# Optimization experiments

Measured on AMD Instinct MI355X. Metric: run time of the kernel, lower is better.

Reference implementation:

```python
import jax, jax.numpy as jnp
import numpy as np
from jax import lax

DN = ('NHWC', 'HWIO', 'NHWC')


def _conv(x, w, b=None, stride=1):
    y = lax.conv_general_dilated(x, w, (stride, stride), 'SAME', dimension_numbers=DN)
    return y + b if b is not None else y


def _conv_t(x, w, b, stride=2):
    y = lax.conv_transpose(x, w, (stride, stride), 'SAME', dimension_numbers=DN)
    return y + b


def _res_stack(x, blocks):
    # ResidualBlock: x + Conv1x1(relu(Conv3x3(relu(x)))); final relu after stack
    for w1, w2 in blocks:
        t = jax.nn.relu(x)
        t = _conv(t, w1)          # 3x3, no bias
        t = jax.nn.relu(t)
        t = _conv(t, w2)          # 1x1, no bias
        x = x + t
    return jax.nn.relu(x)


def setup_inputs() -> dict:
    key = jax.random.key(0)
    ks = jax.random.split(key, 32)
    s = 0.05
    n = lambda i, shape: jax.random.normal(ks[i], shape, dtype=jnp.float32) * s
    H, RH, D, K = 128, 32, 128, 512
    return {
        'x': jax.random.normal(ks[0], (16, 256, 256, 3), dtype=jnp.float32),
        'emb': jax.random.normal(ks[1], (K, D), dtype=jnp.float32),  # stddev 1.0 init
        'enc_w1': n(2, (4, 4, 3, H // 2)),  'enc_b1': jnp.zeros((H // 2,), jnp.float32),
        'enc_w2': n(3, (4, 4, H // 2, H)),  'enc_b2': jnp.zeros((H,), jnp.float32),
        'enc_w3': n(4, (3, 3, H, H)),       'enc_b3': jnp.zeros((H,), jnp.float32),
        'erb1_w1': n(5, (3, 3, H, RH)), 'erb1_w2': n(6, (1, 1, RH, H)),
        'erb2_w1': n(7, (3, 3, H, RH)), 'erb2_w2': n(8, (1, 1, RH, H)),
        'dec_w': n(9, (3, 3, D, H)),        'dec_b': jnp.zeros((H,), jnp.float32),
        'drb1_w1': n(10, (3, 3, H, RH)), 'drb1_w2': n(11, (1, 1, RH, H)),
        'drb2_w1': n(12, (3, 3, H, RH)), 'drb2_w2': n(13, (1, 1, RH, H)),
        'dt1_w': n(14, (4, 4, H, H // 2)),  'dt1_b': jnp.zeros((H // 2,), jnp.float32),
        'dt2_w': n(15, (4, 4, H // 2, 3)),  'dt2_b': jnp.zeros((3,), jnp.float32),
    }


def _forward(x, emb, enc_w1, enc_b1, enc_w2, enc_b2, enc_w3, enc_b3,
             erb1_w1, erb1_w2, erb2_w1, erb2_w2,
             dec_w, dec_b, drb1_w1, drb1_w2, drb2_w1, drb2_w2,
             dt1_w, dt1_b, dt2_w, dt2_b):
    f = jax.nn.relu(_conv(x, enc_w1, enc_b1, 2))
    f = jax.nn.relu(_conv(f, enc_w2, enc_b2, 2))
    f = _conv(f, enc_w3, enc_b3, 1)
    f = _res_stack(f, [(erb1_w1, erb1_w2), (erb2_w1, erb2_w2)])
    # VQ: full [N, K] squared-distance matrix, argmin, codebook gather
    D = emb.shape[1]
    flat = f.reshape(-1, D)                                   # [N, D]
    dist = ((flat ** 2).sum(axis=1, keepdims=True)
            + (emb ** 2).sum(axis=1)[None, :]
            - 2.0 * flat @ emb.T)                              # [N, K]
    idx = jnp.argmin(dist, axis=1)                             # [N]
    q = emb[idx].reshape(f.shape)                              # quantized
    y = _conv(q, dec_w, dec_b, 1)
    y = _res_stack(y, [(drb1_w1, drb1_w2), (drb2_w1, drb2_w2)])
    y = jax.nn.relu(_conv_t(y, dt1_w, dt1_b))
    y = _conv_t(y, dt2_w, dt2_b)
    return (y, f, q)


def reference(x, emb, enc_w1, enc_b1, enc_w2, enc_b2, enc_w3, enc_b3,
              erb1_w1, erb1_w2, erb2_w1, erb2_w2,
              dec_w, dec_b, drb1_w1, drb1_w2, drb2_w1, drb2_w2,
              dt1_w, dt1_b, dt2_w, dt2_b):
    return _forward(x, emb, enc_w1, enc_b1, enc_w2, enc_b2, enc_w3, enc_b3,
                    erb1_w1, erb1_w2, erb2_w1, erb2_w2,
                    dec_w, dec_b, drb1_w1, drb1_w2, drb2_w1, drb2_w2,
                    dt1_w, dt1_b, dt2_w, dt2_b)
```

## Files before the change

kernel.cpp:

```cpp
#include <hip/hip_runtime.h>
#include <hip/hip_bf16.h>
#include <hip/hip_fp16.h>

using bf16 = __hip_bfloat16;
using frag_ab = __attribute__((ext_vector_type(8))) short;
using f16x8  = __attribute__((ext_vector_type(8))) _Float16;
using hf16x2 = __attribute__((ext_vector_type(2))) __fp16;
using frag_cd = __attribute__((ext_vector_type(4))) float;

enum { F_INRELU = 1, F_OUTRELU = 2, F_RES = 4 };

struct TapSet { int dy[16]; int dx[16]; int wi[16]; };

__device__ __forceinline__ unsigned int relu_pk(unsigned int v) {
    unsigned int m = ((v & 0x80008000u) >> 15) * 0xFFFFu;
    return v & ~m;
}
__device__ __forceinline__ unsigned int mask_by(unsigned int v, unsigned int h) {
    unsigned int m = ((h & 0x80008000u) >> 15) * 0xFFFFu;
    return v & ~m;
}
__device__ __forceinline__ int xcd_swz(int bx, int n) {
    return (bx & 7) * (n >> 3) + (bx >> 3);
}

__global__ void pack_w_k(const float* __restrict__ w, bf16* __restrict__ dst,
                         int Ci, int Co, int BN, TapSet taps, int total)
{
    int idx = blockIdx.x * 256 + threadIdx.x;
    if (idx >= total) return;
    int j  = idx & 7;
    int r1 = idx >> 3;
    int nl = r1 % BN;
    int r2 = r1 / BN;
    int q  = r2 & 3;
    int cb = r2 >> 2;
    int nblocks = Co / BN;
    int c  = cb / nblocks;
    int nb = cb - c * nblocks;
    int cpt = Ci >> 5;
    int tap = c / cpt;
    int ci  = (c - tap * cpt) * 32 + q * 8 + j;
    int n   = nb * BN + nl;
    dst[idx] = __float2bfloat16(w[(size_t)(taps.wi[tap] * Ci + ci) * Co + n]);
}

__global__ void pack_w2_k(const float* __restrict__ w, __half* __restrict__ dst,
                          int Ci, int Co, int BN, TapSet taps, int total)
{
    int idx = blockIdx.x * 256 + threadIdx.x;
    if (idx >= total) return;
    int j  = idx & 7;
    int r1 = idx >> 3;
    int nl = r1 % BN;
    int r2 = r1 / BN;
    int q  = r2 & 3;
    int cb = r2 >> 2;
    int nblocks = Co / BN;
    int c  = cb / nblocks;
    int nb = cb - c * nblocks;
    int cpt = Ci >> 5;
    int tap = c / cpt;
    int ci  = (c - tap * cpt) * 32 + q * 8 + j;
    int n   = nb * BN + nl;
    float v = w[(size_t)(taps.wi[tap] * Ci + ci) * Co + n];
    __half h = __float2half(v);
    __half l = __float2half((v - __half2float(h)) * 2048.0f);
    size_t base = (size_t)cb * (BN * 64) + (q * BN + nl) * 8 + j;
    dst[base] = h;
    dst[base + BN * 32] = l;
}

__global__ void pack_wdt2_k(const float* __restrict__ w, __half* __restrict__ dst)
{
    int idx = blockIdx.x * 256 + threadIdx.x;
    if (idx >= 16384) return;
    int parity = idx >> 12;
    int r0 = idx & 4095;
    int j  = r0 & 7;
    int r1 = r0 >> 3;
    int nl = r1 & 15;
    int r2 = r1 >> 4;
    int q  = r2 & 3;
    int cb = r2 >> 2;
    int tap = cb >> 1;
    int cc  = cb & 1;
    int ci  = cc * 32 + q * 8 + j;
    int n   = nl;
    int py = parity >> 1, px = parity & 1;
    int ty = tap >> 1, tx = tap & 1;
    int wi = (py + 2 * ty) * 4 + (px + 2 * tx);
    float v = (n < 3) ? w[(size_t)(wi * 64 + ci) * 3 + n] : 0.f;
    __half h = __float2half(v);
    __half l = __float2half((v - __half2float(h)) * 2048.0f);
    size_t base = (size_t)parity * 8192 + cb * 1024 + (q * 16 + nl) * 8 + j;
    dst[base] = h;
    dst[base + 512] = l;
}

__global__ void pack_we1_k(const float* __restrict__ w, __half* __restrict__ dst)
{
    int idx = blockIdx.x * 256 + threadIdx.x;
    if (idx >= 4096) return;
    int j  = idx & 7;
    int r1 = idx >> 3;
    int nl = r1 & 63;
    int r2 = r1 >> 6;
    int q  = r2 & 3;
    int c  = r2 >> 2;
    int k  = c * 32 + q * 8 + j;
    int tap = k >> 2, ci = k & 3;
    float v = (ci < 3) ? w[(size_t)(tap * 3 + ci) * 64 + nl] : 0.f;
    __half h = __float2half(v);
    __half l = __float2half((v - __half2float(h)) * 2048.0f);
    size_t base = (size_t)c * 4096 + (q * 64 + nl) * 8 + j;
    dst[base] = h;
    dst[base + 2048] = l;
}

__global__ __launch_bounds__(256) void pad_x_k(
    const float* __restrict__ x, __half* __restrict__ xh, __half* __restrict__ xl)
{
    int pix = blockIdx.x * 256 + threadIdx.x;
    const float* ip = x + (size_t)pix * 3;
    float v0 = ip[0], v1 = ip[1], v2 = ip[2];
    unsigned short hb[4], lb[4];
    float vv[4] = {v0, v1, v2, 0.f};
#pragma unroll
    for (int i = 0; i < 4; ++i) {
        __half h = __float2half(vv[i]);
        hb[i] = __half_as_ushort(h);
        lb[i] = __half_as_ushort(__float2half((vv[i] - __half2float(h)) * 2048.0f));
    }
    uint2 hv = make_uint2((unsigned)hb[0] | ((unsigned)hb[1] << 16),
                          (unsigned)hb[2] | ((unsigned)hb[3] << 16));
    uint2 lv = make_uint2((unsigned)lb[0] | ((unsigned)lb[1] << 16),
                          (unsigned)lb[2] | ((unsigned)lb[3] << 16));
    *(uint2*)(xh + (size_t)pix * 4) = hv;
    *(uint2*)(xl + (size_t)pix * 4) = lv;
}

__global__ __launch_bounds__(256) void enc1_mfma_k(
    const __half* __restrict__ xh, const __half* __restrict__ xl,
    const __half* __restrict__ wp, const float* __restrict__ bias,
    __half* __restrict__ oh, __half* __restrict__ ol)
{
    __shared__ __align__(16) short Ash[64 * 32];
    __shared__ __align__(16) short Asl[64 * 32];
    __shared__ __align__(16) short Bsh[64 * 32];
    __shared__ __align__(16) short Bsl[64 * 32];

    const int tid = threadIdx.x;
    const int m0 = xcd_swz(blockIdx.x, 4096) * 64;

    const int am = tid >> 2;
    const int aq = tid & 3;
    const int gm  = m0 + am;
    const int nn_ = gm >> 14;
    const int rr_ = gm & 16383;
    const int iy0 = (rr_ >> 7) * 2 - 1;
    const int ix0 = (rr_ & 127) * 2 - 1;

    const int lane = tid & 63;
    const int wv4 = tid >> 6;
    const int wm = (wv4 & 1) * 32;
    const int wn = (wv4 >> 1) * 32;
    const int lm = lane & 15, lq = lane >> 4;

    frag_cd accA[2][2], accB[2][2];
#pragma unroll
    for (int i = 0; i < 2; ++i)
#pragma unroll
        for (int j = 0; j < 2; ++j)
#pragma unroll
            for (int r = 0; r < 4; ++r) { accA[i][j][r] = 0.f; accB[i][j][r] = 0.f; }

#pragma unroll
    for (int c = 0; c < 2; ++c) {
        const int tap = c * 8 + aq * 2;
        const int ky = tap >> 2, kx = tap & 3;
        const int iy = iy0 + ky;
        const int ix = ix0 + kx;
        uint2 h0 = make_uint2(0u, 0u), h1 = h0, l0 = h0, l1 = h0;
        if (iy >= 0 && iy < 256) {
            const size_t rowb = (size_t)(nn_ * 256 + iy) * 256;
            if (ix >= 0 && ix < 256) {
                h0 = *(const uint2*)(xh + (rowb + ix) * 4);
                l0 = *(const uint2*)(xl + (rowb + ix) * 4);
            }
            if (ix + 1 >= 0 && ix + 1 < 256) {
                h1 = *(const uint2*)(xh + (rowb + ix + 1) * 4);
                l1 = *(const uint2*)(xl + (rowb + ix + 1) * 4);
            }
        }
        __syncthreads();
        *(uint4*)&Ash[(aq * 64 + am) * 8] = make_uint4(h0.x, h0.y, h1.x, h1.y);
        *(uint4*)&Asl[(aq * 64 + am) * 8] = make_uint4(l0.x, l0.y, l1.x, l1.y);
        {
            const __half* wc = wp + (size_t)c * 4096;
            *(uint4*)&Bsh[tid * 8] = *(const uint4*)(wc + tid * 8);
            *(uint4*)&Bsl[tid * 8] = *(const uint4*)(wc + 2048 + tid * 8);
        }
        __syncthreads();

        f16x8 afh[2], afl[2], bfh[2], bfl[2];
#pragma unroll
        for (int i = 0; i < 2; ++i) {
            afh[i] = *(const f16x8*)&Ash[(lq * 64 + wm + i * 16 + lm) * 8];
            afl[i] = *(const f16x8*)&Asl[(lq * 64 + wm + i * 16 + lm) * 8];
        }
#pragma unroll
        for (int j = 0; j < 2; ++j) {
            bfh[j] = *(const f16x8*)&Bsh[(lq * 64 + wn + j * 16 + lm) * 8];
            bfl[j] = *(const f16x8*)&Bsl[(lq * 64 + wn + j * 16 + lm) * 8];
        }
#pragma unroll
        for (int i = 0; i < 2; ++i)
#pragma unroll
            for (int j = 0; j < 2; ++j) {
                accA[i][j] = __builtin_amdgcn_mfma_f32_16x16x32_f16(afh[i], bfh[j], accA[i][j], 0, 0, 0);
                accB[i][j] = __builtin_amdgcn_mfma_f32_16x16x32_f16(afh[i], bfl[j], accB[i][j], 0, 0, 0);
                accB[i][j] = __builtin_amdgcn_mfma_f32_16x16x32_f16(afl[i], bfh[j], accB[i][j], 0, 0, 0);
            }
    }

    const float s = 1.0f / 2048.0f;
#pragma unroll
    for (int j = 0; j < 2; ++j) {
        const int n_g = wn + j * 16 + lm;
        const float bv = bias[n_g];
#pragma unroll
        for (int i = 0; i < 2; ++i) {
#pragma unroll
            for (int r = 0; r < 4; ++r) {
                const int m_g = m0 + wm + i * 16 + lq * 4 + r;
                const size_t ob = (size_t)m_g * 64 + n_g;
                float v = accA[i][j][r] + accB[i][j][r] * s + bv;
                v = fmaxf(v, 0.f);
                __half h = __float2half(v);
                oh[ob] = h;
                ol[ob] = __float2half((v - __half2float(h)) * 2048.0f);
            }
        }
    }
}

template<int BN>
__global__ __launch_bounds__(256) void conv_mfma2_k(
    const __half* __restrict__ ah, const __half* __restrict__ al,
    const __half* __restrict__ wp, const float* __restrict__ bias,
    float* __restrict__ out, __half* __restrict__ oh, __half* __restrict__ ol,
    const __half* __restrict__ rh, const __half* __restrict__ rl,
    int IH, int IW, int Ci, int Co, int sy_in,
    TapSet taps, int ntaps, int flags)
{
    __shared__ __align__(16) short Ash[64 * 32];
    __shared__ __align__(16) short Asl[64 * 32];
    __shared__ __align__(16) short Bsh[BN * 32];
    __shared__ __align__(16) short Bsl[BN * 32];

    const int tid = threadIdx.x;
    const int m0 = xcd_swz(blockIdx.x, gridDim.x) * 64;
    const int n0 = blockIdx.y * BN;

    const int am = tid >> 2;
    const int aq = tid & 3;
    const int gm  = m0 + am;
    const int nn_ = gm >> 12;
    const int rr_ = gm & 4095;
    const int oy_ = (rr_ >> 6) * sy_in;
    const int ox_ = (rr_ & 63) * sy_in;

    const int lane = tid & 63;
    const int wv4 = tid >> 6;
    constexpr int MT = (BN >= 64) ? 2 : 1;
    constexpr int NT = (BN == 128) ? 4 : 2;
    const int wm = (BN >= 64) ? (wv4 & 1) * 32 : wv4 * 16;
    const int wn = (BN == 128) ? (wv4 >> 1) * 64 : ((BN == 64) ? (wv4 >> 1) * 32 : 0);
    const int lm = lane & 15, lq = lane >> 4;
    constexpr int NLOAD = BN * 32 / 8;

    frag_cd accA[MT][NT], accB[MT][NT];
#pragma unroll
    for (int i = 0; i < MT; ++i)
#pragma unroll
        for (int j = 0; j < NT; ++j)
#pragma unroll
            for (int r = 0; r < 4; ++r) { accA[i][j][r] = 0.f; accB[i][j][r] = 0.f; }

    const int cpt = Ci >> 5;
    const int nch = ntaps * cpt;
    const bool inrelu = (flags & F_INRELU) != 0;

    int tap = 0, cc = 0, ci0 = 0;
    for (int c = 0; c < nch; ++c) {
        const int iy = oy_ + taps.dy[tap];
        const int ix = ox_ + taps.dx[tap];
        uint4 avh = make_uint4(0u, 0u, 0u, 0u);
        uint4 avl = make_uint4(0u, 0u, 0u, 0u);
        if (iy >= 0 && iy < IH && ix >= 0 && ix < IW) {
            const size_t off = (size_t)((nn_ * IH + iy) * IW + ix) * Ci + ci0 + aq * 8;
            avh = *(const uint4*)(ah + off);
            avl = *(const uint4*)(al + off);
        }
        if (inrelu) {
            avl.x = mask_by(avl.x, avh.x); avl.y = mask_by(avl.y, avh.y);
            avl.z = mask_by(avl.z, avh.z); avl.w = mask_by(avl.w, avh.w);
            avh.x = relu_pk(avh.x); avh.y = relu_pk(avh.y);
            avh.z = relu_pk(avh.z); avh.w = relu_pk(avh.w);
        }
        uint4 bvh0, bvl0, bvh1, bvl1;
        {
            const __half* wc = wp + (size_t)(c * gridDim.y + blockIdx.y) * (BN * 64);
            if constexpr (BN == 128) {
                bvh0 = *(const uint4*)(wc + tid * 8);
                bvh1 = *(const uint4*)(wc + (256 + tid) * 8);
                bvl0 = *(const uint4*)(wc + BN * 32 + tid * 8);
                bvl1 = *(const uint4*)(wc + BN * 32 + (256 + tid) * 8);
            } else if (tid < NLOAD) {
                bvh0 = *(const uint4*)(wc + tid * 8);
                bvl0 = *(const uint4*)(wc + BN * 32 + tid * 8);
            }
        }

        __syncthreads();
        *(uint4*)&Ash[(aq * 64 + am) * 8] = avh;
        *(uint4*)&Asl[(aq * 64 + am) * 8] = avl;
        if constexpr (BN == 128) {
            *(uint4*)&Bsh[tid * 8] = bvh0;
            *(uint4*)&Bsh[(256 + tid) * 8] = bvh1;
            *(uint4*)&Bsl[tid * 8] = bvl0;
            *(uint4*)&Bsl[(256 + tid) * 8] = bvl1;
        } else if (tid < NLOAD) {
            *(uint4*)&Bsh[tid * 8] = bvh0;
            *(uint4*)&Bsl[tid * 8] = bvl0;
        }
        __syncthreads();

        f16x8 afh[MT], afl[MT], bfh[NT], bfl[NT];
#pragma unroll
        for (int i = 0; i < MT; ++i) {
            afh[i] = *(const f16x8*)&Ash[(lq * 64 + wm + i * 16 + lm) * 8];
            afl[i] = *(const f16x8*)&Asl[(lq * 64 + wm + i * 16 + lm) * 8];
        }
#pragma unroll
        for (int j = 0; j < NT; ++j) {
            bfh[j] = *(const f16x8*)&Bsh[(lq * BN + wn + j * 16 + lm) * 8];
            bfl[j] = *(const f16x8*)&Bsl[(lq * BN + wn + j * 16 + lm) * 8];
        }
#pragma unroll
        for (int i = 0; i < MT; ++i)
#pragma unroll
            for (int j = 0; j < NT; ++j) {
                accA[i][j] = __builtin_amdgcn_mfma_f32_16x16x32_f16(afh[i], bfh[j], accA[i][j], 0, 0, 0);
                accB[i][j] = __builtin_amdgcn_mfma_f32_16x16x32_f16(afh[i], bfl[j], accB[i][j], 0, 0, 0);
                accB[i][j] = __builtin_amdgcn_mfma_f32_16x16x32_f16(afl[i], bfh[j], accB[i][j], 0, 0, 0);
            }

        ci0 += 32;
        if (++cc == cpt) { cc = 0; ci0 = 0; ++tap; }
    }

    const float s = 1.0f / 2048.0f;
#pragma unroll
    for (int j = 0; j < NT; ++j) {
        const int n_g = n0 + wn + j * 16 + lm;
        const float bv = bias ? bias[n_g] : 0.f;
#pragma unroll
        for (int i = 0; i < MT; ++i) {
#pragma unroll
            for (int r = 0; r < 4; ++r) {
                const int m_g = m0 + wm + i * 16 + lq * 4 + r;
                const size_t ob = (size_t)m_g * Co + n_g;
                float v = accA[i][j][r] + accB[i][j][r] * s + bv;
                if (flags & F_RES)
                    v += __half2float(rh[ob]) + __half2float(rl[ob]) * s;
                if (flags & F_OUTRELU) v = fmaxf(v, 0.f);
                if (out) out[ob] = v;
                if (oh) {
                    __half h = __float2half(v);
                    oh[ob] = h;
                    ol[ob] = __float2half((v - __half2float(h)) * 2048.0f);
                }
            }
        }
    }
}

template<int BN>
__global__ __launch_bounds__(256) void conv_mfma_k(
    const bf16* __restrict__ a, const bf16* __restrict__ wp,
    const float* __restrict__ bias,
    float* __restrict__ out, bf16* __restrict__ out_bf,
    const float* __restrict__ res,
    int Ci, int Co, int OHf, int OWf, int sy_out, int py, int px,
    TapSet taps, int ntaps, int flags)
{
    __shared__ __align__(16) short As[64 * 32];
    __shared__ __align__(16) short Bs[BN * 32];

    const int tid = threadIdx.x;
    const int m0 = xcd_swz(blockIdx.x, gridDim.x) * 64;
    const int n0 = blockIdx.y * BN;

    const int am = tid >> 2;
    const int aq = tid & 3;
    const int gm  = m0 + am;
    const int nn_ = gm >> 12;
    const int rr_ = gm & 4095;
    const int oy_ = rr_ >> 6;
    const int ox_ = rr_ & 63;

    const int lane = tid & 63;
    const int wv4 = tid >> 6;
    constexpr int MT = (BN >= 64) ? 2 : 1;
    constexpr int NT = (BN == 128) ? 4 : 2;
    const int wm = (BN >= 64) ? (wv4 & 1) * 32 : wv4 * 16;
    const int wn = (BN == 128) ? (wv4 >> 1) * 64 : ((BN == 64) ? (wv4 >> 1) * 32 : 0);
    const int lm = lane & 15, lq = lane >> 4;
    constexpr int NLOAD = BN * 32 / 8;

    frag_cd acc[MT][NT];
#pragma unroll
    for (int i = 0; i < MT; ++i)
#pragma unroll
        for (int j = 0; j < NT; ++j)
#pragma unroll
            for (int r = 0; r < 4; ++r) acc[i][j][r] = 0.f;

    const int cpt = Ci >> 5;
    const int nch = ntaps * cpt;
    const bool inrelu = (flags & F_INRELU) != 0;

    int tap = 0, cc = 0, ci0 = 0;
    for (int c = 0; c < nch; ++c) {
        const int iy = oy_ + taps.dy[tap];
        const int ix = ox_ + taps.dx[tap];
        uint4 av = make_uint4(0u, 0u, 0u, 0u);
        if (iy >= 0 && iy < 64 && ix >= 0 && ix < 64)
            av = *(const uint4*)(a + (size_t)((nn_ * 64 + iy) * 64 + ix) * Ci + ci0 + aq * 8);
        if (inrelu) {
            av.x = relu_pk(av.x); av.y = relu_pk(av.y);
            av.z = relu_pk(av.z); av.w = relu_pk(av.w);
        }
        uint4 bv0, bv1;
        {
            const bf16* wc = wp + ((size_t)c * gridDim.y + blockIdx.y) * (BN * 32);
            if constexpr (BN == 128) {
                bv0 = *(const uint4*)(wc + tid * 8);
                bv1 = *(const uint4*)(wc + (256 + tid) * 8);
            } else if (tid < NLOAD) {
                bv0 = *(const uint4*)(wc + tid * 8);
            }
        }

        __syncthreads();
        *(uint4*)&As[(aq * 64 + am) * 8] = av;
        if constexpr (BN == 128) {
            *(uint4*)&Bs[tid * 8] = bv0;
            *(uint4*)&Bs[(256 + tid) * 8] = bv1;
        } else if (tid < NLOAD) {
            *(uint4*)&Bs[tid * 8] = bv0;
        }
        __syncthreads();

        frag_ab af[MT], bfr[NT];
#pragma unroll
        for (int i = 0; i < MT; ++i)
            af[i] = *(const frag_ab*)&As[(lq * 64 + wm + i * 16 + lm) * 8];
#pragma unroll
        for (int j = 0; j < NT; ++j)
            bfr[j] = *(const frag_ab*)&Bs[(lq * BN + wn + j * 16 + lm) * 8];
#pragma unroll
        for (int i = 0; i < MT; ++i)
#pragma unroll
            for (int j = 0; j < NT; ++j)
                acc[i][j] = __builtin_amdgcn_mfma_f32_16x16x32_bf16(af[i], bfr[j], acc[i][j], 0, 0, 0);

        ci0 += 32;
        if (++cc == cpt) { cc = 0; ci0 = 0; ++tap; }
    }

#pragma unroll
    for (int j = 0; j < NT; ++j) {
        const int n_g = n0 + wn + j * 16 + lm;
        const float bv = bias ? bias[n_g] : 0.f;
#pragma unroll
        for (int i = 0; i < MT; ++i) {
#pragma unroll
            for (int r = 0; r < 4; ++r) {
                const int m_g = m0 + wm + i * 16 + lq * 4 + r;
                const int nn2 = m_g >> 12;
                const int rr2 = m_g & 4095;
                const int oy = (rr2 >> 6) * sy_out + py;
                const int ox = (rr2 & 63) * sy_out + px;
                const size_t ob = ((size_t)(nn2 * OHf + oy) * OWf + ox) * Co + n_g;
                float v = acc[i][j][r] + bv;
                if (flags & F_RES)     v += res[ob];
                if (flags & F_OUTRELU) v = fmaxf(v, 0.f);
                if (out)    out[ob]    = v;
                if (out_bf) out_bf[ob] = __float2bfloat16(v);
            }
        }
    }
}

__global__ __launch_bounds__(256) void dt2_mfma_k(
    const float* __restrict__ in,
    const __half* __restrict__ wp,
    const float* __restrict__ bias,
    float* __restrict__ out)
{
    __shared__ __align__(16) short Ash[2][64 * 32];
    __shared__ __align__(16) short Bsh[2][16 * 32];
    __shared__ __align__(16) short Bsl[2][16 * 32];

    const int tid = threadIdx.x;
    const int bx  = xcd_swz(blockIdx.x, 16384);
    const int par = bx & 3;
    const int m0  = (bx >> 2) * 64;
    const int py = par >> 1, px = par & 1;

    const int am = tid >> 2;
    const int aq = tid & 3;
    const int gm  = m0 + am;
    const int nn_ = gm >> 14;
    const int rr_ = gm & 16383;
    const int r_  = rr_ >> 7;
    const int c_  = rr_ & 127;

    const int lane = tid & 63;
    const int wv4 = tid >> 6;
    const int wm = wv4 * 16;
    const int lm = lane & 15, lq = lane >> 4;

    frag_cd accA, accB;
#pragma unroll
    for (int r = 0; r < 4; ++r) { accA[r] = 0.f; accB[r] = 0.f; }

    const __half* wpar = wp + (size_t)par * 8192;

    for (int t = 0; t < 4; ++t) {
        const int iy = r_ + py + (t >> 1) - 1;
        const int ix = c_ + px + (t & 1) - 1;
        uint4 hi0 = make_uint4(0u, 0u, 0u, 0u), hi1 = hi0;
        if ((unsigned)iy < 128u && (unsigned)ix < 128u) {
            const float* ip = in + (size_t)((nn_ * 128 + iy) * 128 + ix) * 64 + aq * 8;
#pragma unroll
            for (int h = 0; h < 2; ++h) {
                const float4 v0 = *(const float4*)(ip + h * 32);
                const float4 v1 = *(const float4*)(ip + h * 32 + 4);
                union { hf16x2 p[4]; uint4 u; } uh;
                uh.p[0] = __builtin_amdgcn_cvt_pkrtz(v0.x, v0.y);
                uh.p[1] = __builtin_amdgcn_cvt_pkrtz(v0.z, v0.w);
                uh.p[2] = __builtin_amdgcn_cvt_pkrtz(v1.x, v1.y);
                uh.p[3] = __builtin_amdgcn_cvt_pkrtz(v1.z, v1.w);
                if (h == 0) hi0 = uh.u; else hi1 = uh.u;
            }
        }
        uint4 bvh, bvl;
        if (tid < 128) {
            const __half* wc = wpar + (size_t)(2 * t + (tid >> 6)) * 1024 + (tid & 63) * 8;
            bvh = *(const uint4*)wc;
            bvl = *(const uint4*)(wc + 512);
        }

        __syncthreads();
        *(uint4*)&Ash[0][(aq * 64 + am) * 8] = hi0;
        *(uint4*)&Ash[1][(aq * 64 + am) * 8] = hi1;
        if (tid < 128) {
            *(uint4*)&Bsh[tid >> 6][(tid & 63) * 8] = bvh;
            *(uint4*)&Bsl[tid >> 6][(tid & 63) * 8] = bvl;
        }
        __syncthreads();

#pragma unroll
        for (int h = 0; h < 2; ++h) {
            const f16x8 afh = *(const f16x8*)&Ash[h][(lq * 64 + wm + lm) * 8];
            const f16x8 bfh = *(const f16x8*)&Bsh[h][(lq * 16 + lm) * 8];
            const f16x8 bfl = *(const f16x8*)&Bsl[h][(lq * 16 + lm) * 8];
            accA = __builtin_amdgcn_mfma_f32_16x16x32_f16(afh, bfh, accA, 0, 0, 0);
            accB = __builtin_amdgcn_mfma_f32_16x16x32_f16(afh, bfl, accB, 0, 0, 0);
        }
    }

    const float s = 1.0f / 2048.0f;
    if (lm < 3) {
        const float bv = bias[lm];
#pragma unroll
        for (int r = 0; r < 4; ++r) {
            const int m_g = m0 + wm + lq * 4 + r;
            const int nn2 = m_g >> 14;
            const int rr2 = m_g & 16383;
            const int oy = (rr2 >> 7) * 2 + py;
            const int ox = (rr2 & 127) * 2 + px;
            out[((size_t)(nn2 * 256 + oy) * 256 + ox) * 3 + lm] = accA[r] + accB[r] * s + bv;
        }
    }
}

__global__ void enorm_k(const float* __restrict__ emb, float* __restrict__ en) {
    int k = blockIdx.x * 256 + threadIdx.x;
    if (k >= 512) return;
    const float4* e = (const float4*)(emb + k * 128);
    float s = 0.f;
    for (int i = 0; i < 32; ++i) {
        float4 v = e[i];
        s += v.x * v.x + v.y * v.y + v.z * v.z + v.w * v.w;
    }
    en[k] = s;
}

__global__ void pack_emb_k(const float* __restrict__ emb, __half* __restrict__ dst)
{
    int idx = blockIdx.x * 256 + threadIdx.x;
    int k = idx & 127;
    int n = idx >> 7;
    float v = emb[idx];
    __half h = __float2half(v);
    __half l = __float2half((v - __half2float(h)) * 2048.0f);
    int nb = n >> 6, nl = n & 63;
    int ch = k >> 5, q = (k >> 3) & 3, j = k & 7;
    size_t base = (size_t)(nb * 4 + ch) * 4096 + (q * 64 + nl) * 8 + j;
    dst[base] = h;
    dst[base + 2048] = l;
}

__global__ __launch_bounds__(256) void vq_mfma_k(
    const __half* __restrict__ fh, const __half* __restrict__ fl,
    const __half* __restrict__ pe, const float* __restrict__ en,
    const float* __restrict__ emb, float* __restrict__ q, bf16* __restrict__ qb)
{
    __shared__ __align__(16) short Ash[64 * 128];
    __shared__ __align__(16) short Asl[64 * 128];
    __shared__ int sel[64];

    const int tid  = threadIdx.x;
    const int pos0 = blockIdx.x * 64;

    {
        const int am = tid >> 2;
        const int aq = tid & 3;
#pragma unroll
        for (int ch = 0; ch < 4; ++ch) {
            const size_t off = (size_t)(pos0 + am) * 128 + ch * 32 + aq * 8;
            uint4 vh = *(const uint4*)(fh + off);
            uint4 vl = *(const uint4*)(fl + off);
            *(uint4*)&Ash[((ch * 4 + aq) * 64 + am) * 8] = vh;
            *(uint4*)&Asl[((ch * 4 + aq) * 64 + am) * 8] = vl;
        }
    }
    __syncthreads();

    const int lane = tid & 63;
    const int w    = tid >> 6;
    const int lm = lane & 15, lq = lane >> 4;
    const int mbase = w * 16;
    const float s = 1.0f / 2048.0f;

    float best[4] = {3.4e38f, 3.4e38f, 3.4e38f, 3.4e38f};
    int   bidx[4] = {0, 0, 0, 0};

    f16x8 ah[4], alv[4];
#pragma unroll
    for (int ch = 0; ch < 4; ++ch) {
        ah[ch]  = *(const f16x8*)&Ash[((ch * 4 + lq) * 64 + mbase + lm) * 8];
        alv[ch] = *(const f16x8*)&Asl[((ch * 4 + lq) * 64 + mbase + lm) * 8];
    }

    for (int nb = 0; nb < 8; ++nb) {
        frag_cd accA[4], accB[4];
#pragma unroll
        for (int j = 0; j < 4; ++j)
#pragma unroll
            for (int r = 0; r < 4; ++r) { accA[j][r] = 0.f; accB[j][r] = 0.f; }

#pragma unroll
        for (int ch = 0; ch < 4; ++ch) {
            const __half* base = pe + (size_t)(nb * 4 + ch) * 4096;
            f16x8 bh[4], bl[4];
#pragma unroll
            for (int j = 0; j < 4; ++j) {
                const int o = (lq * 64 + j * 16 + lm) * 8;
                bh[j] = *(const f16x8*)(base + o);
                bl[j] = *(const f16x8*)(base + 2048 + o);
            }
#pragma unroll
            for (int j = 0; j < 4; ++j) {
                accA[j] = __builtin_amdgcn_mfma_f32_16x16x32_f16(ah[ch], bh[j], accA[j], 0, 0, 0);
                accB[j] = __builtin_amdgcn_mfma_f32_16x16x32_f16(ah[ch], bl[j], accB[j], 0, 0, 0);
                accB[j] = __builtin_amdgcn_mfma_f32_16x16x32_f16(alv[ch], bh[j], accB[j], 0, 0, 0);
            }
        }

#pragma unroll
        for (int j = 0; j < 4; ++j) {
            const int code = nb * 64 + j * 16 + lm;
            const float ec = en[code];
#pragma unroll
            for (int r = 0; r < 4; ++r) {
                float dot = accA[j][r] + accB[j][r] * s;
                float d = fmaf(dot, -2.f, ec);
                if (d < best[r]) { best[r] = d; bidx[r] = code; }
            }
        }
    }

#pragma unroll
    for (int r = 0; r < 4; ++r) {
        float d = best[r]; int ix = bidx[r];
#pragma unroll
        for (int m = 1; m < 16; m <<= 1) {
            float d2 = __shfl_xor(d, m);
            int   x2 = __shfl_xor(ix, m);
            if (d2 < d || (d2 == d && x2 < ix)) { d = d2; ix = x2; }
        }
        if (lm == 0) sel[mbase + lq * 4 + r] = ix;
    }
    __syncthreads();

#pragma unroll
    for (int jj = 0; jj < 32; ++jj) {
        int id = jj * 256 + tid;
        int p = id >> 7, k = id & 127;
        float v = emb[(size_t)sel[p] * 128 + k];
        q[(size_t)(pos0 + p) * 128 + k]  = v;
        qb[(size_t)(pos0 + p) * 128 + k] = __float2bfloat16(v);
    }
}

static TapSet conv_taps(int KH, int KW, int pad) {
    TapSet t{};
    for (int ky = 0; ky < KH; ++ky)
        for (int kx = 0; kx < KW; ++kx) {
            int i = ky * KW + kx;
            t.dy[i] = ky - pad; t.dx[i] = kx - pad; t.wi[i] = i;
        }
    return t;
}

static TapSet convt_taps(int py, int px) {
    TapSet t{};
    for (int ty = 0; ty < 2; ++ty)
        for (int tx = 0; tx < 2; ++tx) {
            int i = ty * 2 + tx;
            t.dy[i] = py + ty - 1;
            t.dx[i] = px + tx - 1;
            t.wi[i] = (py + 2 * ty) * 4 + (px + 2 * tx);
        }
    return t;
}

extern "C" void kernel_launch(void* const* d_in, const int* in_sizes, int n_in,
                              void* d_out, int out_size, void* d_ws, size_t ws_size,
                              hipStream_t stream)
{
    const float* x       = (const float*)d_in[0];
    const float* emb     = (const float*)d_in[1];
    const float* enc_w1  = (const float*)d_in[2];
    const float* enc_b1  = (const float*)d_in[3];
    const float* enc_w2  = (const float*)d_in[4];
    const float* enc_b2  = (const float*)d_in[5];
    const float* enc_w3  = (const float*)d_in[6];
    const float* enc_b3  = (const float*)d_in[7];
    const float* erb1_w1 = (const float*)d_in[8];
    const float* erb1_w2 = (const float*)d_in[9];
    const float* erb2_w1 = (const float*)d_in[10];
    const float* erb2_w2 = (const float*)d_in[11];
    const float* dec_w   = (const float*)d_in[12];
    const float* dec_b   = (const float*)d_in[13];
    const float* drb1_w1 = (const float*)d_in[14];
    const float* drb1_w2 = (const float*)d_in[15];
    const float* drb2_w1 = (const float*)d_in[16];
    const float* drb2_w2 = (const float*)d_in[17];
    const float* dt1_w   = (const float*)d_in[18];
    const float* dt1_b   = (const float*)d_in[19];
    const float* dt2_w   = (const float*)d_in[20];
    const float* dt2_b   = (const float*)d_in[21];

    char* wsb = (char*)d_ws;
    __half* H1 = (__half*)wsb;
    __half* L1 = (__half*)(wsb + (size_t)33554432);
    __half* H2 = (__half*)(wsb + (size_t)67108864);
    __half* L2 = (__half*)(wsb + (size_t)83886080);
    __half* Xh = (__half*)(wsb + (size_t)67108864);
    __half* Xl = (__half*)(wsb + (size_t)75497472);
    __half* H3 = (__half*)wsb;
    __half* L3 = (__half*)(wsb + (size_t)16777216);
    __half* H4 = (__half*)(wsb + (size_t)33554432);
    __half* L4 = (__half*)(wsb + (size_t)50331648);
    __half* Ht = (__half*)(wsb + (size_t)100663296);
    __half* Lt = (__half*)(wsb + (size_t)104857600);
    float*  EN = (float*)(wsb + (size_t)109051904);
    __half* Fh = (__half*)wsb;
    __half* Fl = (__half*)(wsb + (size_t)16777216);
    bf16* Qb  = (bf16*)(wsb + (size_t)67108864);
    bf16* Db  = (bf16*)(wsb + (size_t)83886080);
    bf16* Y1b = Qb;
    bf16* Y2b = Db;
    bf16* Tb  = (bf16*)(wsb + (size_t)100663296);
    float* Y0 = (float*)wsb;
    float* Y1 = (float*)(wsb + (size_t)33554432);
    float* A1 = (float*)wsb;
    char* pk = wsb + (size_t)109056000;
    bf16* Pdec  = (bf16*)pk;  pk += 147456 * 2;
    bf16* Pd1w1 = (bf16*)pk;  pk += 36864 * 2;
    bf16* Pd1w2 = (bf16*)pk;  pk += 4096 * 2;
    bf16* Pd2w1 = (bf16*)pk;  pk += 36864 * 2;
    bf16* Pd2w2 = (bf16*)pk;  pk += 4096 * 2;
    bf16* Pdt1[4];
    for (int i = 0; i < 4; ++i) { Pdt1[i] = (bf16*)pk; pk += 65536 * 2; }
    __half* P2enc2 = (__half*)pk; pk += 131072 * 4;
    __half* P2enc3 = (__half*)pk; pk += 147456 * 4;
    __half* P2e1w1 = (__half*)pk; pk += 36864 * 4;
    __half* P2e1w2 = (__half*)pk; pk += 4096 * 4;
    __half* P2e2w1 = (__half*)pk; pk += 36864 * 4;
    __half* P2e2w2 = (__half*)pk; pk += 4096 * 4;
    __half* Pe     = (__half*)pk; pk += 131072 * 2;
    __half* Pe1    = (__half*)pk; pk += 8192 * 2;
    __half* Pdt2   = (__half*)pk; pk += 32768 * 2;

    float* outY = (float*)d_out;
    float* outF = outY + 3145728;
    float* outQ = outF + 8388608;

    const TapSet t3 = conv_taps(3, 3, 1);
    const TapSet t4 = conv_taps(4, 4, 1);
    const TapSet t1 = conv_taps(1, 1, 0);
    TapSet tdt[4];
    for (int p = 0; p < 4; ++p) tdt[p] = convt_taps(p >> 1, p & 1);

    enorm_k<<<2, 256, 0, stream>>>(emb, EN);
    pack_emb_k<<<256, 256, 0, stream>>>(emb, Pe);
    pack_we1_k<<<16, 256, 0, stream>>>(enc_w1, Pe1);
    pack_wdt2_k<<<64, 256, 0, stream>>>(dt2_w, Pdt2);

    pack_w_k<<<(147456 + 255) / 256, 256, 0, stream>>>(dec_w, Pdec, 128, 128, 128, t3, 147456);
    pack_w_k<<<(36864 + 255) / 256, 256, 0, stream>>>(drb1_w1, Pd1w1, 128, 32, 32, t3, 36864);
    pack_w_k<<<(4096 + 255) / 256, 256, 0, stream>>>(drb1_w2, Pd1w2, 32, 128, 128, t1, 4096);
    pack_w_k<<<(36864 + 255) / 256, 256, 0, stream>>>(drb2_w1, Pd2w1, 128, 32, 32, t3, 36864);
    pack_w_k<<<(4096 + 255) / 256, 256, 0, stream>>>(drb2_w2, Pd2w2, 32, 128, 128, t1, 4096);
    for (int p = 0; p < 4; ++p)
        pack_w_k<<<(65536 + 255) / 256, 256, 0, stream>>>(dt1_w, Pdt1[p], 128, 64, 64, tdt[p], 65536);
    pack_w2_k<<<(131072 + 255) / 256, 256, 0, stream>>>(enc_w2, P2enc2, 64, 128, 128, t4, 131072);
    pack_w2_k<<<(147456 + 255) / 256, 256, 0, stream>>>(enc_w3, P2enc3, 128, 128, 128, t3, 147456);
    pack_w2_k<<<(36864 + 255) / 256, 256, 0, stream>>>(erb1_w1, P2e1w1, 128, 32, 32, t3, 36864);
    pack_w2_k<<<(4096 + 255) / 256, 256, 0, stream>>>(erb1_w2, P2e1w2, 32, 128, 128, t1, 4096);
    pack_w2_k<<<(36864 + 255) / 256, 256, 0, stream>>>(erb2_w1, P2e2w1, 128, 32, 32, t3, 36864);
    pack_w2_k<<<(4096 + 255) / 256, 256, 0, stream>>>(erb2_w2, P2e2w2, 32, 128, 128, t1, 4096);

    pad_x_k<<<4096, 256, 0, stream>>>(x, Xh, Xl);
    enc1_mfma_k<<<4096, 256, 0, stream>>>(Xh, Xl, Pe1, enc_b1, H1, L1);
    conv_mfma2_k<128><<<dim3(1024, 1), 256, 0, stream>>>(H1, L1, P2enc2, enc_b2,
        nullptr, H2, L2, nullptr, nullptr, 128, 128, 64, 128, 2, t4, 16, F_OUTRELU);
    conv_mfma2_k<128><<<dim3(1024, 1), 256, 0, stream>>>(H2, L2, P2enc3, enc_b3,
        nullptr, H3, L3, nullptr, nullptr, 64, 64, 128, 128, 1, t3, 9, 0);
    conv_mfma2_k<32><<<dim3(1024, 1), 256, 0, stream>>>(H3, L3, P2e1w1, nullptr,
        nullptr, Ht, Lt, nullptr, nullptr, 64, 64, 128, 32, 1, t3, 9, F_INRELU);
    conv_mfma2_k<128><<<dim3(1024, 1), 256, 0, stream>>>(Ht, Lt, P2e1w2, nullptr,
        nullptr, H4, L4, H3, L3, 64, 64, 32, 128, 1, t1, 1, F_INRELU | F_RES);
    conv_mfma2_k<32><<<dim3(1024, 1), 256, 0, stream>>>(H4, L4, P2e2w1, nullptr,
        nullptr, Ht, Lt, nullptr, nullptr, 64, 64, 128, 32, 1, t3, 9, F_INRELU);
    conv_mfma2_k<128><<<dim3(1024, 1), 256, 0, stream>>>(Ht, Lt, P2e2w2, nullptr,
        outF, Fh, Fl, H4, L4, 64, 64, 32, 128, 1, t1, 1, F_INRELU | F_RES | F_OUTRELU);

    vq_mfma_k<<<1024, 256, 0, stream>>>(Fh, Fl, Pe, EN, emb, outQ, Qb);

    conv_mfma_k<128><<<dim3(1024, 1), 256, 0, stream>>>(Qb, Pdec, dec_b, Y0, Db, nullptr,
        128, 128, 64, 64, 1, 0, 0, t3, 9, 0);
    conv_mfma_k<32><<<dim3(1024, 1), 256, 0, stream>>>(Db, Pd1w1, nullptr, nullptr, Tb, nullptr,
        128, 32, 64, 64, 1, 0, 0, t3, 9, F_INRELU);
    conv_mfma_k<128><<<dim3(1024, 1), 256, 0, stream>>>(Tb, Pd1w2, nullptr, Y1, Y1b, Y0,
        32, 128, 64, 64, 1, 0, 0, t1, 1, F_INRELU | F_RES);
    conv_mfma_k<32><<<dim3(1024, 1), 256, 0, stream>>>(Y1b, Pd2w1, nullptr, nullptr, Tb, nullptr,
        128, 32, 64, 64, 1, 0, 0, t3, 9, F_INRELU);
    conv_mfma_k<128><<<dim3(1024, 1), 256, 0, stream>>>(Tb, Pd2w2, nullptr, nullptr, Y2b, Y1,
        32, 128, 64, 64, 1, 0, 0, t1, 1, F_INRELU | F_RES | F_OUTRELU);
    for (int p = 0; p < 4; ++p)
        conv_mfma_k<64><<<dim3(1024, 1), 256, 0, stream>>>(Y2b, Pdt1[p], dt1_b, A1, nullptr, nullptr,
            128, 64, 128, 128, 2, p >> 1, p & 1, tdt[p], 4, F_OUTRELU);

    dt2_mfma_k<<<16384, 256, 0, stream>>>(A1, Pdt2, dt2_b, outY);
}
```

Measured before the change: 802.9 us.

## Fuse decoder residual block 3x3 and 1x1 convs into one kernel

Adds a kernel that computes each decoder residual block in one pass. It runs the 3x3 conv (128->32) with input ReLU, keeps the ReLU'd 32-channel intermediate in shared memory as bf16, then applies the 1x1 conv (32->128) with the residual add and optional output ReLU. This replaces four kernel launches with two and removes the global write and read of the intermediate tensor. The cost is a single-buffered K loop with two barriers per step and a small per-block tile (64x32), which may give poor latency hiding compared with the generic conv kernel.

```diff
diff --git a/kernel.cpp b/kernel.cpp
--- a/kernel.cpp
+++ b/kernel.cpp
@@ -505,6 +505,105 @@
     }
 }
 
+__global__ __launch_bounds__(256) void dres_k(
+    const bf16* __restrict__ a,
+    const bf16* __restrict__ w3,
+    const bf16* __restrict__ w1,
+    const float* __restrict__ res,
+    float* __restrict__ out,
+    bf16* __restrict__ out_bf,
+    TapSet taps, int outrelu)
+{
+    __shared__ __align__(16) short As[64 * 32];
+    __shared__ __align__(16) short Bs[32 * 32];
+    __shared__ __align__(16) short Bs2[32 * 128];
+    __shared__ bf16 Tsh[64 * 32];
+
+    const int tid = threadIdx.x;
+    const int m0 = xcd_swz(blockIdx.x, gridDim.x) * 64;
+
+    const int am = tid >> 2;
+    const int aq = tid & 3;
+    const int gm  = m0 + am;
+    const int nn_ = gm >> 12;
+    const int rr_ = gm & 4095;
+    const int oy_ = rr_ >> 6;
+    const int ox_ = rr_ & 63;
+
+    const int lane = tid & 63;
+    const int wv4 = tid >> 6;
+    const int wm = wv4 * 16;
+    const int lm = lane & 15, lq = lane >> 4;
+
+    *(uint4*)&Bs2[tid * 8] = *(const uint4*)(w1 + tid * 8);
+    *(uint4*)&Bs2[(256 + tid) * 8] = *(const uint4*)(w1 + (256 + tid) * 8);
+
+    frag_cd acc[2];
+#pragma unroll
+    for (int j = 0; j < 2; ++j)
+#pragma unroll
+        for (int r = 0; r < 4; ++r) acc[j][r] = 0.f;
+
+    for (int c = 0; c < 36; ++c) {
+        const int tap = c >> 2;
+        const int ci0 = (c & 3) * 32;
+        const int iy = oy_ + taps.dy[tap];
+        const int ix = ox_ + taps.dx[tap];
+        uint4 av = make_uint4(0u, 0u, 0u, 0u);
+        if (iy >= 0 && iy < 64 && ix >= 0 && ix < 64)
+            av = *(const uint4*)(a + (size_t)((nn_ * 64 + iy) * 64 + ix) * 128 + ci0 + aq * 8);
+        av.x = relu_pk(av.x); av.y = relu_pk(av.y);
+        av.z = relu_pk(av.z); av.w = relu_pk(av.w);
+        uint4 bv;
+        if (tid < 128)
+            bv = *(const uint4*)(w3 + (size_t)c * 1024 + tid * 8);
+
+        __syncthreads();
+        *(uint4*)&As[(aq * 64 + am) * 8] = av;
+        if (tid < 128) *(uint4*)&Bs[tid * 8] = bv;
+        __syncthreads();
+
+        const frag_ab af = *(const frag_ab*)&As[(lq * 64 + wm + lm) * 8];
+#pragma unroll
+        for (int j = 0; j < 2; ++j) {
+            const frag_ab bfr = *(const frag_ab*)&Bs[(lq * 32 + j * 16 + lm) * 8];
+            acc[j] = __builtin_amdgcn_mfma_f32_16x16x32_bf16(af, bfr, acc[j], 0, 0, 0);
+        }
+    }
+
+#pragma unroll
+    for (int j = 0; j < 2; ++j)
+#pragma unroll
+        for (int r = 0; r < 4; ++r)
+            Tsh[(wm + lq * 4 + r) * 32 + j * 16 + lm] =
+                __float2bfloat16(fmaxf(acc[j][r], 0.f));
+    __syncthreads();
+
+    const frag_ab af2 = *(const frag_ab*)&Tsh[(wm + lm) * 32 + lq * 8];
+    frag_cd acc2[8];
+#pragma unroll
+    for (int j = 0; j < 8; ++j) {
+#pragma unroll
+        for (int r = 0; r < 4; ++r) acc2[j][r] = 0.f;
+        const frag_ab bfr2 = *(const frag_ab*)&Bs2[(lq * 128 + j * 16 + lm) * 8];
+        acc2[j] = __builtin_amdgcn_mfma_f32_16x16x32_bf16(af2, bfr2, acc2[j], 0, 0, 0);
+    }
+
+#pragma unroll
+    for (int j = 0; j < 8; ++j) {
+        const int n_g = j * 16 + lm;
+#pragma unroll
+        for (int r = 0; r < 4; ++r) {
+            const int m_g = m0 + wm + lq * 4 + r;
+            const size_t ob = (size_t)m_g * 128 + n_g;
+            float v = acc2[j][r] + res[ob];
+            if (outrelu) v = fmaxf(v, 0.f);
+            if (out) out[ob] = v;
+            out_bf[ob] = __float2bfloat16(v);
+        }
+    }
+}
+
 __global__ __launch_bounds__(256) void dt2_mfma_k(
     const float* __restrict__ in,
     const __half* __restrict__ wp,
@@ -798,7 +897,6 @@
     bf16* Db  = (bf16*)(wsb + (size_t)83886080);
     bf16* Y1b = Qb;
     bf16* Y2b = Db;
-    bf16* Tb  = (bf16*)(wsb + (size_t)100663296);
     float* Y0 = (float*)wsb;
     float* Y1 = (float*)(wsb + (size_t)33554432);
     float* A1 = (float*)wsb;
@@ -868,14 +966,8 @@
 
     conv_mfma_k<128><<<dim3(1024, 1), 256, 0, stream>>>(Qb, Pdec, dec_b, Y0, Db, nullptr,
         128, 128, 64, 64, 1, 0, 0, t3, 9, 0);
-    conv_mfma_k<32><<<dim3(1024, 1), 256, 0, stream>>>(Db, Pd1w1, nullptr, nullptr, Tb, nullptr,
-        128, 32, 64, 64, 1, 0, 0, t3, 9, F_INRELU);
-    conv_mfma_k<128><<<dim3(1024, 1), 256, 0, stream>>>(Tb, Pd1w2, nullptr, Y1, Y1b, Y0,
-        32, 128, 64, 64, 1, 0, 0, t1, 1, F_INRELU | F_RES);
-    conv_mfma_k<32><<<dim3(1024, 1), 256, 0, stream>>>(Y1b, Pd2w1, nullptr, nullptr, Tb, nullptr,
-        128, 32, 64, 64, 1, 0, 0, t3, 9, F_INRELU);
-    conv_mfma_k<128><<<dim3(1024, 1), 256, 0, stream>>>(Tb, Pd2w2, nullptr, nullptr, Y2b, Y1,
-        32, 128, 64, 64, 1, 0, 0, t1, 1, F_INRELU | F_RES | F_OUTRELU);
+    dres_k<<<1024, 256, 0, stream>>>(Db, Pd1w1, Pd1w2, Y0, Y1, Y1b, t3, 0);
+    dres_k<<<1024, 256, 0, stream>>>(Y1b, Pd2w1, Pd2w2, Y1, nullptr, Y2b, t3, 1);
     for (int p = 0; p < 4; ++p)
         conv_mfma_k<64><<<dim3(1024, 1), 256, 0, stream>>>(Y2b, Pdt1[p], dt1_b, A1, nullptr, nullptr,
             128, 64, 128, 128, 2, p >> 1, p & 1, tdt[p], 4, F_OUTRELU);
```

Measured after the change: 789.6 us. No clear change (-1.6%).
